# Performance work log

Hardware: AMD Instinct MI355X
Metric: run time of the kernel (lower is better)

Reference implementation:

```python
import jax, jax.numpy as jnp
import numpy as np

NUM_HEADS = 12


def setup_inputs() -> dict:
    key = jax.random.key(0)
    ks = jax.random.split(key, 8)
    B, Nq, Nk, C = 4, 2048, 2048, 768
    s = 0.02
    return {
        "query": jax.random.normal(ks[0], (B, Nq, C), dtype=jnp.float32),
        "key": jax.random.normal(ks[1], (B, Nk, C), dtype=jnp.float32),
        "value": jax.random.normal(ks[2], (B, Nk, C), dtype=jnp.float32),
        "Wq": jax.random.normal(ks[3], (C, C), dtype=jnp.float32) * s,
        "Wk": jax.random.normal(ks[4], (C, C), dtype=jnp.float32) * s,
        "Wv": jax.random.normal(ks[5], (C, C), dtype=jnp.float32) * s,
        "Wo": jax.random.normal(ks[6], (C, C), dtype=jnp.float32) * s,
        "bo": jnp.zeros((C,), dtype=jnp.float32),
    }


def reference(query, key, value, Wq, Wk, Wv, Wo, bo):
    B, Nq, C = query.shape
    Nk = key.shape[1]
    H = NUM_HEADS
    Dh = C // H
    scale = Dh ** -0.5
    # nn.Linear: x @ W.T ; split heads -> [B, H, N, Dh]
    q = (query @ Wq.T).reshape(B, Nq, H, Dh).transpose(0, 2, 1, 3)
    k = (key @ Wk.T).reshape(B, Nk, H, Dh).transpose(0, 2, 1, 3)
    v = (value @ Wv.T).reshape(B, Nk, H, Dh).transpose(0, 2, 1, 3)
    # attention logits [B, H, Nq, Nk]
    attn = jnp.einsum("bhqd,bhkd->bhqk", q, k) * scale
    attn = jax.nn.softmax(attn, axis=-1)
    x = jnp.einsum("bhqk,bhkd->bhqd", attn, v)  # [B, H, Nq, Dh]
    x = x.transpose(0, 2, 1, 3).reshape(B, Nq, C)
    return x @ Wo.T + bo
```

## Files before the change

kernel.cpp:

```cpp
#include <hip/hip_runtime.h>
#include <hip/hip_bf16.h>
#include <stdint.h>

typedef unsigned short u16;
typedef unsigned int   u32;
typedef unsigned long long u64;

typedef __attribute__((ext_vector_type(8)))  short short8;
typedef __attribute__((ext_vector_type(4)))  u32   u32x4;
typedef __attribute__((ext_vector_type(4)))  float f32x4;
typedef __attribute__((ext_vector_type(16))) float f32x16;


__device__ __forceinline__ u16 f2bf(float f) {
  u32 u = __builtin_bit_cast(u32, f);
  u += 0x7FFFu + ((u >> 16) & 1u);
  return (u16)(u >> 16);
}

__device__ __forceinline__ void gload16(const void* g, void* l) {
  __builtin_amdgcn_global_load_lds((__attribute__((address_space(1))) void*)(g),
                                   (__attribute__((address_space(3))) void*)(l),
                                   16, 0, 0);
}

__device__ __forceinline__ u32 cvtpk(float lo, float hi) {
  u32 r;
  asm("v_cvt_pk_bf16_f32 %0, %1, %2" : "=v"(r) : "v"(lo), "v"(hi));
  return r;
}


__global__ __launch_bounds__(256)
void cvt3_kernel(const float* __restrict__ a, const float* __restrict__ b,
                 const float* __restrict__ c, u16* __restrict__ oa,
                 u16* __restrict__ ob, u16* __restrict__ oc, int n4) {
  int i = blockIdx.x * 256 + threadIdx.x;
  if (i >= n4) return;
  const float* in = blockIdx.y == 0 ? a : blockIdx.y == 1 ? b : c;
  u16* out = blockIdx.y == 0 ? oa : blockIdx.y == 1 ? ob : oc;
  float4 v = reinterpret_cast<const float4*>(in)[i];
  u64 pk = (u64)f2bf(v.x) | ((u64)f2bf(v.y) << 16)
         | ((u64)f2bf(v.z) << 32) | ((u64)f2bf(v.w) << 48);
  reinterpret_cast<u64*>(out)[i] = pk;
}

__global__ __launch_bounds__(256)
void cvtw_kernel(const float* __restrict__ Wq, const float* __restrict__ Wk,
                 const float* __restrict__ Wv, const float* __restrict__ Wo,
                 u16* __restrict__ Wcat, u16* __restrict__ WoB, int n4, float qs) {
  int i = blockIdx.x * 256 + threadIdx.x;
  if (i >= n4) return;
  int y = blockIdx.y;
  const float* in = y == 0 ? Wq : y == 1 ? Wk : y == 2 ? Wv : Wo;
  u16* out = y == 0 ? Wcat : y == 1 ? (Wcat + 589824) : y == 2 ? (Wcat + 1179648) : WoB;
  float s = y == 0 ? qs : 1.f;
  float4 v = reinterpret_cast<const float4*>(in)[i];
  u64 pk = (u64)f2bf(v.x * s) | ((u64)f2bf(v.y * s) << 16)
         | ((u64)f2bf(v.z * s) << 32) | ((u64)f2bf(v.w * s) << 48);
  reinterpret_cast<u64*>(out)[i] = pk;
}

template<int MODE>
__global__ __launch_bounds__(256)
void gemm128(const u16* __restrict__ Aq, const u16* __restrict__ Ak,
             const u16* __restrict__ Av, const u16* __restrict__ Bw,
             u16* __restrict__ Cqk, u16* __restrict__ Vt,
             float* __restrict__ Cout, const float* __restrict__ bias) {
  constexpr int K  = 768;
  constexpr int KT = K / 32;
  __shared__ char lds[32768];
  char* A0 = lds;          char* A1 = lds + 8192;
  char* B0 = lds + 16384;  char* B1 = lds + 24576;

  const int tid = threadIdx.x, lane = tid & 63, wid = tid >> 6;
  const int bm = blockIdx.x, bn = blockIdx.y;
  const int wr = wid >> 1, wc = wid & 1;

  const u16* Abase = Aq;
  if constexpr (MODE == 0) Abase = (bn < 6) ? Aq : (bn < 12) ? Ak : Av;

  const char* Ag = (const char*)Abase + (size_t)bm * 128 * (K * 2);
  const char* Bg = (const char*)Bw    + (size_t)bn * 128 * (K * 2);

  f32x4 acc[4][4];
  #pragma unroll
  for (int m = 0; m < 4; ++m)
    #pragma unroll
    for (int n = 0; n < 4; ++n)
      #pragma unroll
      for (int r = 0; r < 4; ++r) acc[m][n][r] = 0.f;

  #pragma unroll
  for (int c = 0; c < 2; ++c) {
    int chunk = c * 4 + wid;
    int off = chunk * 1024 + lane * 16;
    int row = off >> 6, colb = off & 63;
    gload16(Ag + (size_t)row * (K * 2) + colb, A0 + chunk * 1024);
    gload16(Bg + (size_t)row * (K * 2) + colb, B0 + chunk * 1024);
  }
  __syncthreads();

  for (int kt = 0; kt < KT; ++kt) {
    const int cur = kt & 1;
    char* Ac = cur ? A1 : A0;  char* Bc = cur ? B1 : B0;
    char* An = cur ? A0 : A1;  char* Bn = cur ? B0 : B1;
    if (kt + 1 < KT) {
      #pragma unroll
      for (int c = 0; c < 2; ++c) {
        int chunk = c * 4 + wid;
        int off = chunk * 1024 + lane * 16;
        int row = off >> 6, colb = off & 63;
        gload16(Ag + (size_t)row * (K * 2) + (kt + 1) * 64 + colb, An + chunk * 1024);
        gload16(Bg + (size_t)row * (K * 2) + (kt + 1) * 64 + colb, Bn + chunk * 1024);
      }
    }
    short8 af[4], bf[4];
    #pragma unroll
    for (int m = 0; m < 4; ++m) {
      int row = wr * 64 + m * 16 + (lane & 15);
      af[m] = *reinterpret_cast<const short8*>(Ac + row * 64 + ((lane >> 4) * 16));
    }
    #pragma unroll
    for (int n = 0; n < 4; ++n) {
      int row = wc * 64 + n * 16 + (lane & 15);
      bf[n] = *reinterpret_cast<const short8*>(Bc + row * 64 + ((lane >> 4) * 16));
    }
    #pragma unroll
    for (int m = 0; m < 4; ++m)
      #pragma unroll
      for (int n = 0; n < 4; ++n)
        acc[m][n] = __builtin_amdgcn_mfma_f32_16x16x32_bf16(af[m], bf[n], acc[m][n], 0, 0, 0);
    __syncthreads();
  }

  if constexpr (MODE == 0) {
    if (bn < 12) {
      #pragma unroll
      for (int m = 0; m < 4; ++m) {
        int grow0 = bm * 128 + wr * 64 + m * 16 + ((lane >> 4) << 2);
        #pragma unroll
        for (int n = 0; n < 4; ++n) {
          int col = bn * 128 + wc * 64 + n * 16 + (lane & 15);
          #pragma unroll
          for (int r = 0; r < 4; ++r)
            Cqk[(size_t)(grow0 + r) * 1536 + col] = f2bf(acc[m][n][r]);
        }
      }
    } else {
      #pragma unroll
      for (int m = 0; m < 4; ++m) {
        int grow0 = bm * 128 + wr * 64 + m * 16 + ((lane >> 4) << 2);
        int bb = grow0 >> 11, nn = grow0 & 2047;
        #pragma unroll
        for (int n = 0; n < 4; ++n) {
          int vc = (bn - 12) * 128 + wc * 64 + n * 16 + (lane & 15);
          int hid = vc >> 6, d = vc & 63;
          u64 pk = (u64)f2bf(acc[m][n][0]) | ((u64)f2bf(acc[m][n][1]) << 16)
                 | ((u64)f2bf(acc[m][n][2]) << 32) | ((u64)f2bf(acc[m][n][3]) << 48);
          *reinterpret_cast<u64*>(Vt + ((size_t)(bb * 12 + hid) * 64 + d) * 2048 + nn) = pk;
        }
      }
    }
  } else {
    #pragma unroll
    for (int m = 0; m < 4; ++m) {
      int grow0 = bm * 128 + wr * 64 + m * 16 + ((lane >> 4) << 2);
      #pragma unroll
      for (int n = 0; n < 4; ++n) {
        int col = bn * 128 + wc * 64 + n * 16 + (lane & 15);
        float bs = bias[col];
        #pragma unroll
        for (int r = 0; r < 4; ++r)
          Cout[(size_t)(grow0 + r) * 768 + col] = acc[m][n][r] + bs;
      }
    }
  }
}

__global__ __launch_bounds__(256)
void attn_fwd(const u16* __restrict__ QK, const u16* __restrict__ Vt,
              u16* __restrict__ X) {
  __shared__ char lds[32768];
  char* K0 = lds;          char* K1 = lds + 8192;
  char* V0 = lds + 16384;  char* V1 = lds + 24576;

  const int tid = threadIdx.x, lane = tid & 63, wid = tid >> 6;
  const int qt = blockIdx.x, bh = blockIdx.y;
  const int b = bh / 12, h = bh - b * 12;
  const int hh = lane >> 5;

  const char* Qg = (const char*)QK + ((size_t)(b * 2048 + qt * 128) * 1536 + h * 64) * 2;
  const char* Kg = (const char*)QK + ((size_t)(b * 2048) * 1536 + 768 + h * 64) * 2;
  const char* Vg = (const char*)Vt + ((size_t)bh * 64 * 2048) * 2;

  const int off0 = wid * 1024 + lane * 16;
  const int off1 = off0 + 4096;
  const int r0 = off0 >> 7, i0 = (off0 & 127) ^ ((r0 & 7) << 4);
  const int r1 = off1 >> 7, i1 = (off1 & 127) ^ ((r1 & 7) << 4);
  const size_t kso0 = (size_t)r0 * 3072 + i0, kso1 = (size_t)r1 * 3072 + i1;
  const size_t vso0 = (size_t)r0 * 4096 + i0, vso1 = (size_t)r1 * 4096 + i1;

  gload16(Kg + kso0, K0 + off0);
  gload16(Kg + kso1, K0 + off1);
  gload16(Vg + vso0, V0 + off0);
  gload16(Vg + vso1, V0 + off1);

  short8 qf[4];
  {
    const char* Qrow = Qg + (size_t)(wid * 32 + (lane & 31)) * 3072 + hh * 16;
    #pragma unroll
    for (int kk = 0; kk < 4; ++kk)
      qf[kk] = *reinterpret_cast<const short8*>(Qrow + kk * 32);
  }
  __syncthreads();

  f32x16 o0, o1;
  #pragma unroll
  for (int r = 0; r < 16; ++r) { o0[r] = 0.f; o1[r] = 0.f; }
  float m_run = -1e30f, l_run = 0.f;

  for (int t = 0; t < 32; ++t) {
    const int cur = t & 1;
    char* Kc = cur ? K1 : K0;  char* Vc = cur ? V1 : V0;
    char* Kn = cur ? K0 : K1;  char* Vn = cur ? V0 : V1;
    if (t + 1 < 32) {
      const char* Kgn = Kg + (size_t)(t + 1) * 64 * 3072;
      const char* Vgn = Vg + (size_t)(t + 1) * 128;
      gload16(Kgn + kso0, Kn + off0);
      gload16(Kgn + kso1, Kn + off1);
      gload16(Vgn + vso0, Vn + off0);
      gload16(Vgn + vso1, Vn + off1);
    }

    f32x16 sa, sb;
    #pragma unroll
    for (int r = 0; r < 16; ++r) { sa[r] = 0.f; sb[r] = 0.f; }
    {
      const int ra = lane & 31;
      const int swa = (ra & 7) << 4;
      const char* Ka = Kc + ra * 128;
      const char* Kb2 = Kc + (32 + ra) * 128;
      __builtin_amdgcn_s_setprio(1);
      #pragma unroll
      for (int kk = 0; kk < 4; ++kk) {
        int inner = (kk * 32 + hh * 16) ^ swa;
        short8 ka = *reinterpret_cast<const short8*>(Ka + inner);
        short8 kb = *reinterpret_cast<const short8*>(Kb2 + inner);
        sa = __builtin_amdgcn_mfma_f32_32x32x16_bf16(ka, qf[kk], sa, 0, 0, 0);
        sb = __builtin_amdgcn_mfma_f32_32x32x16_bf16(kb, qf[kk], sb, 0, 0, 0);
      }
      __builtin_amdgcn_s_setprio(0);
    }

    float mx = fmaxf(sa[0], sa[1]);
    #pragma unroll
    for (int r = 2; r < 16; r += 2) mx = fmaxf(fmaxf(mx, sa[r]), sa[r + 1]);
    #pragma unroll
    for (int r = 0; r < 16; r += 2) mx = fmaxf(fmaxf(mx, sb[r]), sb[r + 1]);
    mx = fmaxf(mx, __shfl_xor(mx, 32));

    if (__any(mx > m_run + 8.f)) {
      const float mnew = fmaxf(m_run, mx);
      const float alpha = __builtin_amdgcn_exp2f(m_run - mnew);
      #pragma unroll
      for (int r = 0; r < 16; ++r) { o0[r] *= alpha; o1[r] *= alpha; }
      l_run *= alpha;
      m_run = mnew;
    }

    float pa[16], pb[16];
    float s0 = 0.f, s1 = 0.f, s2 = 0.f, s3 = 0.f;
    #pragma unroll
    for (int r = 0; r < 16; r += 4) {
      pa[r]     = __builtin_amdgcn_exp2f(sa[r]     - m_run); s0 += pa[r];
      pa[r + 1] = __builtin_amdgcn_exp2f(sa[r + 1] - m_run); s1 += pa[r + 1];
      pa[r + 2] = __builtin_amdgcn_exp2f(sa[r + 2] - m_run); s2 += pa[r + 2];
      pa[r + 3] = __builtin_amdgcn_exp2f(sa[r + 3] - m_run); s3 += pa[r + 3];
    }
    #pragma unroll
    for (int r = 0; r < 16; r += 4) {
      pb[r]     = __builtin_amdgcn_exp2f(sb[r]     - m_run); s0 += pb[r];
      pb[r + 1] = __builtin_amdgcn_exp2f(sb[r + 1] - m_run); s1 += pb[r + 1];
      pb[r + 2] = __builtin_amdgcn_exp2f(sb[r + 2] - m_run); s2 += pb[r + 2];
      pb[r + 3] = __builtin_amdgcn_exp2f(sb[r + 3] - m_run); s3 += pb[r + 3];
    }
    float rs = (s0 + s1) + (s2 + s3);
    rs += __shfl_xor(rs, 32);
    l_run += rs;

    short8 pf[4];
    {
      u32 ca[8], cb[8];
      #pragma unroll
      for (int i = 0; i < 8; ++i) {
        ca[i] = cvtpk(pa[2 * i], pa[2 * i + 1]);
        cb[i] = cvtpk(pb[2 * i], pb[2 * i + 1]);
      }
      #pragma unroll
      for (int i = 0; i < 2; ++i) {
        u32 e0 = (u32)__shfl_xor((int)(hh ? ca[4 * i + 0] : ca[4 * i + 2]), 32);
        u32 e1 = (u32)__shfl_xor((int)(hh ? ca[4 * i + 1] : ca[4 * i + 3]), 32);
        u32x4 w = hh ? (u32x4){e0, e1, ca[4 * i + 2], ca[4 * i + 3]}
                     : (u32x4){ca[4 * i + 0], ca[4 * i + 1], e0, e1};
        pf[i] = __builtin_bit_cast(short8, w);
      }
      #pragma unroll
      for (int i = 0; i < 2; ++i) {
        u32 e0 = (u32)__shfl_xor((int)(hh ? cb[4 * i + 0] : cb[4 * i + 2]), 32);
        u32 e1 = (u32)__shfl_xor((int)(hh ? cb[4 * i + 1] : cb[4 * i + 3]), 32);
        u32x4 w = hh ? (u32x4){e0, e1, cb[4 * i + 2], cb[4 * i + 3]}
                     : (u32x4){cb[4 * i + 0], cb[4 * i + 1], e0, e1};
        pf[2 + i] = __builtin_bit_cast(short8, w);
      }
    }

    {
      const int rv = lane & 31;
      const int swv = (rv & 7) << 4;
      const char* Va = Vc + rv * 128;
      const char* Vb = Vc + (32 + rv) * 128;
      __builtin_amdgcn_s_setprio(1);
      #pragma unroll
      for (int st = 0; st < 4; ++st) {
        int inner = (st * 32 + hh * 16) ^ swv;
        short8 v0 = *reinterpret_cast<const short8*>(Va + inner);
        short8 v1 = *reinterpret_cast<const short8*>(Vb + inner);
        o0 = __builtin_amdgcn_mfma_f32_32x32x16_bf16(v0, pf[st], o0, 0, 0, 0);
        o1 = __builtin_amdgcn_mfma_f32_32x32x16_bf16(v1, pf[st], o1, 0, 0, 0);
      }
      __builtin_amdgcn_s_setprio(0);
    }
    __syncthreads();
  }

  const float invl = __builtin_amdgcn_rcpf(l_run);
  const int q = qt * 128 + wid * 32 + (lane & 31);
  u16* Xp = X + (size_t)(b * 2048 + q) * 768;
  #pragma unroll
  for (int mt = 0; mt < 2; ++mt) {
    #pragma unroll
    for (int rr = 0; rr < 4; ++rr) {
      float e0 = (mt ? o1[rr * 4 + 0] : o0[rr * 4 + 0]) * invl;
      float e1 = (mt ? o1[rr * 4 + 1] : o0[rr * 4 + 1]) * invl;
      float e2 = (mt ? o1[rr * 4 + 2] : o0[rr * 4 + 2]) * invl;
      float e3 = (mt ? o1[rr * 4 + 3] : o0[rr * 4 + 3]) * invl;
      int col = h * 64 + mt * 32 + 8 * rr + 4 * hh;
      u64 pk = (u64)f2bf(e0) | ((u64)f2bf(e1) << 16)
             | ((u64)f2bf(e2) << 32) | ((u64)f2bf(e3) << 48);
      *reinterpret_cast<u64*>(Xp + col) = pk;
    }
  }
}


extern "C" void kernel_launch(void* const* d_in, const int* in_sizes, int n_in,
                              void* d_out, int out_size, void* d_ws, size_t ws_size,
                              hipStream_t stream) {
  const float* query = (const float*)d_in[0];
  const float* key   = (const float*)d_in[1];
  const float* value = (const float*)d_in[2];
  const float* Wq    = (const float*)d_in[3];
  const float* Wk    = (const float*)d_in[4];
  const float* Wv    = (const float*)d_in[5];
  const float* Wo    = (const float*)d_in[6];
  const float* bo    = (const float*)d_in[7];

  char* ws = (char*)d_ws;
  u16* Wcat = (u16*)ws;
  u16* WoB  = (u16*)(ws + (size_t)2304 * 768 * 2);
  u16* Xq   = (u16*)(ws + (size_t)2304 * 768 * 2 + (size_t)768 * 768 * 2);
  u16* Xk   = Xq  + (size_t)8192 * 768;
  u16* Xv   = Xk  + (size_t)8192 * 768;
  u16* QKb  = Xv  + (size_t)8192 * 768;
  u16* VtB  = QKb + (size_t)8192 * 1536;

  const float qs = 0.125f * 1.4426950408889634f;
  cvtw_kernel<<<dim3(576, 4), 256, 0, stream>>>(Wq, Wk, Wv, Wo, Wcat, WoB, 147456, qs);
  cvt3_kernel<<<dim3(6144, 3), 256, 0, stream>>>(query, key, value, Xq, Xk, Xv, 1572864);

  gemm128<0><<<dim3(64, 18), 256, 0, stream>>>(Xq, Xk, Xv, Wcat, QKb, VtB, nullptr, nullptr);
  attn_fwd<<<dim3(16, 48), 256, 0, stream>>>(QKb, VtB, Xq);
  gemm128<1><<<dim3(64, 6), 256, 0, stream>>>(Xq, nullptr, nullptr, WoB, nullptr, nullptr,
                                              (float*)d_out, bo);
}
```

Measured before the change: 178.0 us.

## Fuse fp32-to-bf16 activation conversion into QKV GEMM and remap blocks across XCDs

```diff
diff --git a/kernel.cpp b/kernel.cpp
--- a/kernel.cpp
+++ b/kernel.cpp
@@ -30,20 +30,6 @@
   return r;
 }
 
-
-__global__ __launch_bounds__(256)
-void cvt3_kernel(const float* __restrict__ a, const float* __restrict__ b,
-                 const float* __restrict__ c, u16* __restrict__ oa,
-                 u16* __restrict__ ob, u16* __restrict__ oc, int n4) {
-  int i = blockIdx.x * 256 + threadIdx.x;
-  if (i >= n4) return;
-  const float* in = blockIdx.y == 0 ? a : blockIdx.y == 1 ? b : c;
-  u16* out = blockIdx.y == 0 ? oa : blockIdx.y == 1 ? ob : oc;
-  float4 v = reinterpret_cast<const float4*>(in)[i];
-  u64 pk = (u64)f2bf(v.x) | ((u64)f2bf(v.y) << 16)
-         | ((u64)f2bf(v.z) << 32) | ((u64)f2bf(v.w) << 48);
-  reinterpret_cast<u64*>(out)[i] = pk;
-}
 
 __global__ __launch_bounds__(256)
 void cvtw_kernel(const float* __restrict__ Wq, const float* __restrict__ Wk,
@@ -63,8 +49,9 @@
 
 template<int MODE>
 __global__ __launch_bounds__(256)
-void gemm128(const u16* __restrict__ Aq, const u16* __restrict__ Ak,
-             const u16* __restrict__ Av, const u16* __restrict__ Bw,
+void gemm128(const float* __restrict__ Af0, const float* __restrict__ Af1,
+             const float* __restrict__ Af2, const u16* __restrict__ Ab,
+             const u16* __restrict__ Bw,
              u16* __restrict__ Cqk, u16* __restrict__ Vt,
              float* __restrict__ Cout, const float* __restrict__ bias) {
   constexpr int K  = 768;
@@ -74,14 +61,26 @@
   char* B0 = lds + 16384;  char* B1 = lds + 24576;
 
   const int tid = threadIdx.x, lane = tid & 63, wid = tid >> 6;
-  const int bm = blockIdx.x, bn = blockIdx.y;
+
+  const int nwg = gridDim.x, cpx = nwg >> 3, hw = blockIdx.x;
+  const int L = (hw & 7) * cpx + (hw >> 3);
+  const int bm = L & 63, bn = L >> 6;
+
   const int wr = wid >> 1, wc = wid & 1;
 
-  const u16* Abase = Aq;
-  if constexpr (MODE == 0) Abase = (bn < 6) ? Aq : (bn < 12) ? Ak : Av;
-
-  const char* Ag = (const char*)Abase + (size_t)bm * 128 * (K * 2);
-  const char* Bg = (const char*)Bw    + (size_t)bn * 128 * (K * 2);
+  const char* Bg = (const char*)Bw + (size_t)bn * 128 * (K * 2);
+
+  const int arow = tid >> 1, ashalf = tid & 1;
+  const float* Agr = nullptr;
+  const char* Ag16 = nullptr;
+  if constexpr (MODE == 0) {
+    const float* Asrc = (bn < 6) ? Af0 : (bn < 12) ? Af1 : Af2;
+    Agr = Asrc + (size_t)(bm * 128 + arow) * 768 + ashalf * 16;
+  } else {
+    Ag16 = (const char*)Ab + (size_t)bm * 128 * (K * 2);
+  }
+  const int wswz = (arow & 3) << 4;
+  const int aswz = (MODE == 0) ? ((lane & 3) << 4) : 0;
 
   f32x4 acc[4][4];
   #pragma unroll
@@ -91,14 +90,54 @@
       #pragma unroll
       for (int r = 0; r < 4; ++r) acc[m][n][r] = 0.f;
 
-  #pragma unroll
-  for (int c = 0; c < 2; ++c) {
-    int chunk = c * 4 + wid;
-    int off = chunk * 1024 + lane * 16;
-    int row = off >> 6, colb = off & 63;
-    gload16(Ag + (size_t)row * (K * 2) + colb, A0 + chunk * 1024);
-    gload16(Bg + (size_t)row * (K * 2) + colb, B0 + chunk * 1024);
-  }
+  float4 areg[4];
+  auto loadA = [&](int kt) {
+    if constexpr (MODE == 0) {
+      #pragma unroll
+      for (int j = 0; j < 4; ++j)
+        areg[j] = *reinterpret_cast<const float4*>(Agr + kt * 32 + 4 * j);
+    }
+  };
+  auto writeA = [&](char* An) {
+    if constexpr (MODE == 0) {
+      u32 c8[8];
+      #pragma unroll
+      for (int j = 0; j < 4; ++j) {
+        c8[2 * j]     = cvtpk(areg[j].x, areg[j].y);
+        c8[2 * j + 1] = cvtpk(areg[j].z, areg[j].w);
+      }
+      char* dst = An + arow * 64;
+      u32x4 w0 = { c8[0], c8[1], c8[2], c8[3] };
+      u32x4 w1 = { c8[4], c8[5], c8[6], c8[7] };
+      *reinterpret_cast<u32x4*>(dst + ((ashalf * 32) ^ wswz))      = w0;
+      *reinterpret_cast<u32x4*>(dst + ((ashalf * 32 + 16) ^ wswz)) = w1;
+    }
+  };
+  auto stageB = [&](char* Bn, int kt) {
+    #pragma unroll
+    for (int c = 0; c < 2; ++c) {
+      int chunk = c * 4 + wid;
+      int off = chunk * 1024 + lane * 16;
+      int row = off >> 6, colb = off & 63;
+      gload16(Bg + (size_t)row * (K * 2) + kt * 64 + colb, Bn + chunk * 1024);
+    }
+  };
+  auto stageA16 = [&](char* An, int kt) {
+    if constexpr (MODE == 1) {
+      #pragma unroll
+      for (int c = 0; c < 2; ++c) {
+        int chunk = c * 4 + wid;
+        int off = chunk * 1024 + lane * 16;
+        int row = off >> 6, colb = off & 63;
+        gload16(Ag16 + (size_t)row * (K * 2) + kt * 64 + colb, An + chunk * 1024);
+      }
+    }
+  };
+
+  loadA(0);
+  stageB(B0, 0);
+  stageA16(A0, 0);
+  writeA(A0);
   __syncthreads();
 
   for (int kt = 0; kt < KT; ++kt) {
@@ -106,31 +145,29 @@
     char* Ac = cur ? A1 : A0;  char* Bc = cur ? B1 : B0;
     char* An = cur ? A0 : A1;  char* Bn = cur ? B0 : B1;
     if (kt + 1 < KT) {
-      #pragma unroll
-      for (int c = 0; c < 2; ++c) {
-        int chunk = c * 4 + wid;
-        int off = chunk * 1024 + lane * 16;
-        int row = off >> 6, colb = off & 63;
-        gload16(Ag + (size_t)row * (K * 2) + (kt + 1) * 64 + colb, An + chunk * 1024);
-        gload16(Bg + (size_t)row * (K * 2) + (kt + 1) * 64 + colb, Bn + chunk * 1024);
-      }
+      loadA(kt + 1);
+      stageB(Bn, kt + 1);
+      stageA16(An, kt + 1);
     }
     short8 af[4], bf[4];
     #pragma unroll
     for (int m = 0; m < 4; ++m) {
       int row = wr * 64 + m * 16 + (lane & 15);
-      af[m] = *reinterpret_cast<const short8*>(Ac + row * 64 + ((lane >> 4) * 16));
+      af[m] = *reinterpret_cast<const short8*>(Ac + row * 64 + (((lane >> 4) * 16) ^ aswz));
     }
     #pragma unroll
     for (int n = 0; n < 4; ++n) {
       int row = wc * 64 + n * 16 + (lane & 15);
       bf[n] = *reinterpret_cast<const short8*>(Bc + row * 64 + ((lane >> 4) * 16));
     }
+    __builtin_amdgcn_s_setprio(1);
     #pragma unroll
     for (int m = 0; m < 4; ++m)
       #pragma unroll
       for (int n = 0; n < 4; ++n)
         acc[m][n] = __builtin_amdgcn_mfma_f32_16x16x32_bf16(af[m], bf[n], acc[m][n], 0, 0, 0);
+    __builtin_amdgcn_s_setprio(0);
+    if (kt + 1 < KT) writeA(An);
     __syncthreads();
   }
 
@@ -186,7 +223,9 @@
   char* V0 = lds + 16384;  char* V1 = lds + 24576;
 
   const int tid = threadIdx.x, lane = tid & 63, wid = tid >> 6;
-  const int qt = blockIdx.x, bh = blockIdx.y;
+  const int hw = blockIdx.x;
+  const int L = (hw & 7) * 96 + (hw >> 3);
+  const int bh = L >> 4, qt = L & 15;
   const int b = bh / 12, h = bh - b * 12;
   const int hh = lane >> 5;
 
@@ -253,6 +292,20 @@
       __builtin_amdgcn_s_setprio(0);
     }
 
+    short8 vreg[8];
+    {
+      const int rv = lane & 31;
+      const int swv = (rv & 7) << 4;
+      const char* Va = Vc + rv * 128;
+      const char* Vb = Vc + (32 + rv) * 128;
+      #pragma unroll
+      for (int st = 0; st < 4; ++st) {
+        int inner = (st * 32 + hh * 16) ^ swv;
+        vreg[2 * st]     = *reinterpret_cast<const short8*>(Va + inner);
+        vreg[2 * st + 1] = *reinterpret_cast<const short8*>(Vb + inner);
+      }
+    }
+
     float mx = fmaxf(sa[0], sa[1]);
     #pragma unroll
     for (int r = 2; r < 16; r += 2) mx = fmaxf(fmaxf(mx, sa[r]), sa[r + 1]);
@@ -315,22 +368,13 @@
       }
     }
 
-    {
-      const int rv = lane & 31;
-      const int swv = (rv & 7) << 4;
-      const char* Va = Vc + rv * 128;
-      const char* Vb = Vc + (32 + rv) * 128;
-      __builtin_amdgcn_s_setprio(1);
-      #pragma unroll
-      for (int st = 0; st < 4; ++st) {
-        int inner = (st * 32 + hh * 16) ^ swv;
-        short8 v0 = *reinterpret_cast<const short8*>(Va + inner);
-        short8 v1 = *reinterpret_cast<const short8*>(Vb + inner);
-        o0 = __builtin_amdgcn_mfma_f32_32x32x16_bf16(v0, pf[st], o0, 0, 0, 0);
-        o1 = __builtin_amdgcn_mfma_f32_32x32x16_bf16(v1, pf[st], o1, 0, 0, 0);
-      }
-      __builtin_amdgcn_s_setprio(0);
-    }
+    __builtin_amdgcn_s_setprio(1);
+    #pragma unroll
+    for (int st = 0; st < 4; ++st) {
+      o0 = __builtin_amdgcn_mfma_f32_32x32x16_bf16(vreg[2 * st],     pf[st], o0, 0, 0, 0);
+      o1 = __builtin_amdgcn_mfma_f32_32x32x16_bf16(vreg[2 * st + 1], pf[st], o1, 0, 0, 0);
+    }
+    __builtin_amdgcn_s_setprio(0);
     __syncthreads();
   }
 
@@ -370,17 +414,15 @@
   u16* Wcat = (u16*)ws;
   u16* WoB  = (u16*)(ws + (size_t)2304 * 768 * 2);
   u16* Xq   = (u16*)(ws + (size_t)2304 * 768 * 2 + (size_t)768 * 768 * 2);
-  u16* Xk   = Xq  + (size_t)8192 * 768;
-  u16* Xv   = Xk  + (size_t)8192 * 768;
-  u16* QKb  = Xv  + (size_t)8192 * 768;
+  u16* QKb  = Xq  + (size_t)8192 * 768 * 3;
   u16* VtB  = QKb + (size_t)8192 * 1536;
 
   const float qs = 0.125f * 1.4426950408889634f;
   cvtw_kernel<<<dim3(576, 4), 256, 0, stream>>>(Wq, Wk, Wv, Wo, Wcat, WoB, 147456, qs);
-  cvt3_kernel<<<dim3(6144, 3), 256, 0, stream>>>(query, key, value, Xq, Xk, Xv, 1572864);
-
-  gemm128<0><<<dim3(64, 18), 256, 0, stream>>>(Xq, Xk, Xv, Wcat, QKb, VtB, nullptr, nullptr);
-  attn_fwd<<<dim3(16, 48), 256, 0, stream>>>(QKb, VtB, Xq);
-  gemm128<1><<<dim3(64, 6), 256, 0, stream>>>(Xq, nullptr, nullptr, WoB, nullptr, nullptr,
-                                              (float*)d_out, bo);
-}
+
+  gemm128<0><<<dim3(1152), 256, 0, stream>>>(query, key, value, nullptr, Wcat,
+                                             QKb, VtB, nullptr, nullptr);
+  attn_fwd<<<dim3(768), 256, 0, stream>>>(QKb, VtB, Xq);
+  gemm128<1><<<dim3(384), 256, 0, stream>>>(nullptr, nullptr, nullptr, Xq, WoB,
+                                            nullptr, nullptr, (float*)d_out, bo);
+}
```

After: 199.2 us. 1.12x slower.
